# Kernel tuning notes

Hardware: AMD Instinct MI355X
Metric: run time of the kernel (lower is better)

## Reference

```python
import jax, jax.numpy as jnp
import numpy as np

N_NODES = 50000
N_EDGES = 800000
IN_DIM = 128
HIDDEN = 256
N_CLASSES = 16
N_GRAPHS = 128


def setup_inputs() -> dict:
    key = jax.random.key(0)
    ks = jax.random.split(key, 10)
    x = jax.random.normal(ks[0], (N_NODES, IN_DIM), dtype=jnp.float32)
    edge_index = jax.random.randint(ks[1], (2, N_EDGES), 0, N_NODES, dtype=jnp.int64)
    batch = jnp.sort(jax.random.randint(ks[2], (N_NODES,), 0, N_GRAPHS, dtype=jnp.int64))
    s = 1.0 / np.sqrt(HIDDEN)
    return {
        "x": x,
        "edge_index": edge_index,
        "batch": batch,
        "W_in": jax.random.normal(ks[3], (IN_DIM, HIDDEN), dtype=jnp.float32) / np.sqrt(IN_DIM),
        "b_in": jnp.zeros((HIDDEN,), dtype=jnp.float32),
        "W1": jax.random.normal(ks[4], (HIDDEN, HIDDEN), dtype=jnp.float32) * s,
        "b1": jnp.zeros((HIDDEN,), dtype=jnp.float32),
        "W2": jax.random.normal(ks[5], (HIDDEN, HIDDEN), dtype=jnp.float32) * s,
        "b2": jnp.zeros((HIDDEN,), dtype=jnp.float32),
        "W_out": jax.random.normal(ks[6], (HIDDEN, N_CLASSES), dtype=jnp.float32) * s,
        "b_out": jnp.zeros((N_CLASSES,), dtype=jnp.float32),
    }


def gcn_conv(x, W, b, src, dst):
    # PyG GCNConv: add self-loops, symmetric norm D^-1/2 A D^-1/2, scatter-add at target.
    h = x @ W  # [N, H]
    n = x.shape[0]
    # degree of target nodes, including one self-loop per node
    deg = jax.ops.segment_sum(jnp.ones_like(dst, dtype=h.dtype), dst, num_segments=n) + 1.0
    dinv = deg ** -0.5  # [N]
    norm = dinv[src] * dinv[dst]  # [E]
    msg = h[src] * norm[:, None]  # [E, H]  gather + scale
    agg = jax.ops.segment_sum(msg, dst, num_segments=n)  # scatter-add
    agg = agg + h * (dinv * dinv)[:, None]  # self-loop contribution
    return agg + b


def reference(x, edge_index, batch, W_in, b_in, W1, b1, W2, b2, W_out, b_out):
    src, dst = edge_index[0], edge_index[1]
    h = x @ W_in + b_in
    # layer 1 (dropout is identity in eval mode)
    h = jax.nn.relu(gcn_conv(h, W1, b1, src, dst))
    # layer 2
    h = jax.nn.relu(gcn_conv(h, W2, b2, src, dst))
    # global mean pool over graphs
    sums = jax.ops.segment_sum(h, batch, num_segments=N_GRAPHS)  # [G, H]
    counts = jax.ops.segment_sum(jnp.ones((h.shape[0],), h.dtype), batch, num_segments=N_GRAPHS)
    pooled = sums / jnp.maximum(counts, 1.0)[:, None]
    return pooled @ W_out + b_out  # [G, n_classes]
```

## Files before the change

### kernel.cpp

```cpp
#include <hip/hip_runtime.h>
#include <hip/hip_bf16.h>

typedef __attribute__((ext_vector_type(8))) short bf16x8;
typedef __attribute__((ext_vector_type(4))) float f32x4;

__device__ __forceinline__ unsigned short f2bf(float f) {
    unsigned u = __float_as_uint(f);
    u += 0x7fff + ((u >> 16) & 1);
    return (unsigned short)(u >> 16);
}
__device__ __forceinline__ float bf2f(unsigned short s) {
    return __uint_as_float(((unsigned)s) << 16);
}

#define GL2LDS16(g, l) __builtin_amdgcn_global_load_lds(                      \
        (const __attribute__((address_space(1))) void*)(g),                   \
        (__attribute__((address_space(3))) void*)(l), 16, 0, 0)


__global__ __launch_bounds__(256) void fused_misc_kernel(
        const int* __restrict__ dst, int* __restrict__ cnt, int e,
        const float* __restrict__ W2, unsigned short* __restrict__ Wt2,
        const float* __restrict__ x, unsigned short* __restrict__ xb, int n4,
        int CB, int TB) {
    int b = blockIdx.x;
    if (b < CB) {
        int i = b * 256 + threadIdx.x;
        if (i < e) atomicAdd(&cnt[dst[i]], 1);
    } else if (b < CB + TB) {
        int i = (b - CB) * 256 + threadIdx.x;
        int k = i >> 8, n = i & 255;
        Wt2[(size_t)n * 256 + k] = f2bf(W2[i]);
    } else {
        int i = (b - CB - TB) * 256 + threadIdx.x;
        if (i < n4) {
            float4 v = ((const float4*)x)[i];
            ushort4 o;
            o.x = f2bf(v.x); o.y = f2bf(v.y); o.z = f2bf(v.z); o.w = f2bf(v.w);
            ((ushort4*)xb)[i] = o;
        }
    }
}


__global__ __launch_bounds__(256) void wfuse_kernel(const float* __restrict__ W_in,
                                                    const float* __restrict__ b_in,
                                                    const float* __restrict__ W1,
                                                    unsigned short* __restrict__ WfT,
                                                    float* __restrict__ bv) {
    __shared__ float row[256];
    int k = blockIdx.x;
    int n = threadIdx.x;
    row[n] = (k < 128) ? W_in[k * 256 + n] : b_in[n];
    __syncthreads();
    float acc = 0.f;
    #pragma unroll 4
    for (int j = 0; j < 256; ++j) acc = fmaf(row[j], W1[j * 256 + n], acc);
    if (k < 128) WfT[(size_t)n * 128 + k] = f2bf(acc);
    else bv[n] = acc;
}


__global__ __launch_bounds__(256) void block_sum_kernel(const int* __restrict__ cnt,
                                                        int* __restrict__ bsums, int n) {
    int tid = threadIdx.x;
    int i = blockIdx.x * 256 + tid;
    int v = (i < n) ? cnt[i] : 0;
    #pragma unroll
    for (int off = 32; off > 0; off >>= 1) v += __shfl_down(v, off);
    __shared__ int ws[4];
    if ((tid & 63) == 0) ws[tid >> 6] = v;
    __syncthreads();
    if (tid == 0) bsums[blockIdx.x] = ws[0] + ws[1] + ws[2] + ws[3];
}

__global__ __launch_bounds__(256) void scatter_scan_kernel(const int* __restrict__ cnt,
                                                           const int* __restrict__ bsums,
                                                           int* __restrict__ offsets,
                                                           int* __restrict__ cursor,
                                                           float* __restrict__ dinv,
                                                           int n, int nb) {
    int tid = threadIdx.x;
    int lane = tid & 63, wid = tid >> 6;
    __shared__ int ws[4], wp[4];

    int bv = (tid < nb && tid < (int)blockIdx.x) ? bsums[tid] : 0;
    int br = bv;
    #pragma unroll
    for (int off = 32; off > 0; off >>= 1) br += __shfl_down(br, off);
    if (lane == 0) wp[wid] = br;

    int i = blockIdx.x * 256 + tid;
    int v = (i < n) ? cnt[i] : 0;
    int s = v;
    #pragma unroll
    for (int off = 1; off < 64; off <<= 1) {
        int t = __shfl_up(s, off);
        if (lane >= off) s += t;
    }
    if (lane == 63) ws[wid] = s;
    __syncthreads();
    int wo = 0;
    #pragma unroll
    for (int k = 0; k < 4; ++k) wo += (k < wid) ? ws[k] : 0;
    int bpref = wp[0] + wp[1] + wp[2] + wp[3];
    int excl = bpref + wo + s - v;
    if (i <= n) { offsets[i] = excl; }
    if (i < n) {
        cursor[i] = excl;
        dinv[i] = rsqrtf((float)v + 1.0f);
    }
}

__global__ void fill_kernel(const int* __restrict__ src, const int* __restrict__ dst,
                            int* __restrict__ cursor, int* __restrict__ csr, int e) {
    int i = blockIdx.x * blockDim.x + threadIdx.x;
    if (i < e) {
        int p = atomicAdd(&cursor[dst[i]], 1);
        csr[p] = src[i];
    }
}


template <int MODE>
__global__ __launch_bounds__(256) void gemm_bf16(const unsigned short* __restrict__ A,
                                                 const unsigned short* __restrict__ Wt,
                                                 const float* __restrict__ aux,
                                                 const float* __restrict__ aux2,
                                                 const float* __restrict__ aux3,
                                                 unsigned short* __restrict__ C,
                                                 int M, int K) {
    __shared__ unsigned short As[128 * 64];
    __shared__ unsigned short Bs[128 * 64];
    const int tid  = threadIdx.x;
    const int lane = tid & 63;
    const int w    = tid >> 6;
    const int wr   = w >> 1, wc = w & 1;
    const int row0 = blockIdx.x * 128;
    const int col0 = blockIdx.y * 128;
    const int mlane = lane & 15, quad = lane >> 4;

    f32x4 acc[4][4];
    #pragma unroll
    for (int i = 0; i < 4; ++i)
        #pragma unroll
        for (int j = 0; j < 4; ++j) acc[i][j] = f32x4{0.f, 0.f, 0.f, 0.f};

    const unsigned short* gA[4]; const unsigned short* gB[4];
    unsigned short* lA[4]; unsigned short* lB[4];
    #pragma unroll
    for (int p = 0; p < 4; ++p) {
        int cid = (p * 4 + w) * 64 + lane;
        int row = cid >> 3, slot = cid & 7;
        int rowA = row0 + row; if (rowA >= M) rowA = M - 1;
        gA[p] = A + (size_t)rowA * K + slot * 8;
        gB[p] = Wt + (size_t)(col0 + row) * K + slot * 8;
        lA[p] = &As[((p * 4 + w) * 64) * 8];
        lB[p] = &Bs[((p * 4 + w) * 64) * 8];
    }

    for (int k0 = 0; k0 < K; k0 += 64) {
        #pragma unroll
        for (int p = 0; p < 4; ++p) GL2LDS16(gA[p] + k0, lA[p]);
        #pragma unroll
        for (int p = 0; p < 4; ++p) GL2LDS16(gB[p] + k0, lB[p]);
        __syncthreads();
        #pragma unroll
        for (int ks = 0; ks < 2; ++ks) {
            bf16x8 af[4], bfv[4];
            #pragma unroll
            for (int i = 0; i < 4; ++i)
                af[i] = *(const bf16x8*)&As[(wr * 64 + i * 16 + mlane) * 64 + ks * 32 + quad * 8];
            #pragma unroll
            for (int j = 0; j < 4; ++j)
                bfv[j] = *(const bf16x8*)&Bs[(wc * 64 + j * 16 + mlane) * 64 + ks * 32 + quad * 8];
            #pragma unroll
            for (int i = 0; i < 4; ++i)
                #pragma unroll
                for (int j = 0; j < 4; ++j)
                    acc[i][j] = __builtin_amdgcn_mfma_f32_16x16x32_bf16(af[i], bfv[j], acc[i][j], 0, 0, 0);
        }
        __syncthreads();
    }

    float bj[4], cj[4];
    if (MODE == 0) {
        #pragma unroll
        for (int j = 0; j < 4; ++j) bj[j] = aux[col0 + wc * 64 + j * 16 + mlane];
    } else if (MODE == 2) {
        #pragma unroll
        for (int j = 0; j < 4; ++j) {
            int gcol = col0 + wc * 64 + j * 16 + mlane;
            bj[j] = aux2[gcol];
            cj[j] = aux3[gcol];
        }
    }
    #pragma unroll
    for (int i = 0; i < 4; ++i) {
        #pragma unroll
        for (int r = 0; r < 4; ++r) {
            int grow = row0 + wr * 64 + i * 16 + quad * 4 + r;
            if (grow < M) {
                float d = (MODE != 0) ? aux[grow] : 0.f;
                #pragma unroll
                for (int j = 0; j < 4; ++j) {
                    int gcol = col0 + wc * 64 + j * 16 + mlane;
                    float v = acc[i][j][r];
                    if (MODE == 0)      v = v + bj[j];
                    else if (MODE == 1) v = v * d;
                    else {              v = fmaf(d, bj[j], v) + cj[j]; v = fmaxf(v, 0.f); }
                    C[(size_t)grow * 256 + gcol] = f2bf(v);
                }
            }
        }
    }
}


__global__ __launch_bounds__(256) void agg_x_kernel(const unsigned short* __restrict__ xb,
                                                    const int* __restrict__ offsets,
                                                    const int* __restrict__ csr,
                                                    const float* __restrict__ dinv,
                                                    unsigned short* __restrict__ ax,
                                                    float* __restrict__ s_out, int n) {
    int node = blockIdx.x * 4 + (threadIdx.x >> 6);
    if (node >= n) return;
    int lane = threadIdx.x & 63;
    int half = lane >> 5, hl = lane & 31;
    const ushort4* x4 = (const ushort4*)xb;
    int beg = offsets[node], end = offsets[node + 1];
    float dn = dinv[node];
    float a0 = 0.f, a1 = 0.f, a2 = 0.f, a3 = 0.f;
    float sdl = 0.f;
    int e = beg;
    while (e < end) {
        int cnt = end - e; if (cnt > 64) cnt = 64;
        int myi = 0; float mydv = 0.f;
        if (lane < cnt) { myi = csr[e + lane]; mydv = dinv[myi]; sdl += mydv; }
        int j = 0;
        for (; j + 8 <= cnt; j += 8) {
            int s0 = __shfl(myi, j + half),     s1 = __shfl(myi, j + 2 + half);
            int s2 = __shfl(myi, j + 4 + half), s3 = __shfl(myi, j + 6 + half);
            float d0 = __shfl(mydv, j + half),     d1 = __shfl(mydv, j + 2 + half);
            float d2 = __shfl(mydv, j + 4 + half), d3 = __shfl(mydv, j + 6 + half);
            ushort4 v0 = x4[(size_t)s0 * 32 + hl];
            ushort4 v1 = x4[(size_t)s1 * 32 + hl];
            ushort4 v2 = x4[(size_t)s2 * 32 + hl];
            ushort4 v3 = x4[(size_t)s3 * 32 + hl];
            a0 = fmaf(bf2f(v0.x), d0, a0); a1 = fmaf(bf2f(v0.y), d0, a1);
            a2 = fmaf(bf2f(v0.z), d0, a2); a3 = fmaf(bf2f(v0.w), d0, a3);
            a0 = fmaf(bf2f(v1.x), d1, a0); a1 = fmaf(bf2f(v1.y), d1, a1);
            a2 = fmaf(bf2f(v1.z), d1, a2); a3 = fmaf(bf2f(v1.w), d1, a3);
            a0 = fmaf(bf2f(v2.x), d2, a0); a1 = fmaf(bf2f(v2.y), d2, a1);
            a2 = fmaf(bf2f(v2.z), d2, a2); a3 = fmaf(bf2f(v2.w), d2, a3);
            a0 = fmaf(bf2f(v3.x), d3, a0); a1 = fmaf(bf2f(v3.y), d3, a1);
            a2 = fmaf(bf2f(v3.z), d3, a2); a3 = fmaf(bf2f(v3.w), d3, a3);
        }
        for (; j < cnt; j += 2) {
            int jj = j + half; int sel = (jj < cnt) ? jj : j;
            int s_ = __shfl(myi, sel);
            float dd = __shfl(mydv, sel);
            if (jj >= cnt) dd = 0.f;
            ushort4 v = x4[(size_t)s_ * 32 + hl];
            a0 = fmaf(bf2f(v.x), dd, a0); a1 = fmaf(bf2f(v.y), dd, a1);
            a2 = fmaf(bf2f(v.z), dd, a2); a3 = fmaf(bf2f(v.w), dd, a3);
        }
        e += cnt;
    }
    a0 += __shfl_xor(a0, 32); a1 += __shfl_xor(a1, 32);
    a2 += __shfl_xor(a2, 32); a3 += __shfl_xor(a3, 32);
    float sd = sdl;
    #pragma unroll
    for (int off = 32; off > 0; off >>= 1) sd += __shfl_down(sd, off);
    if (lane < 32) {
        ushort4 sv = x4[(size_t)node * 32 + hl];
        a0 = fmaf(dn, bf2f(sv.x), a0) * dn;
        a1 = fmaf(dn, bf2f(sv.y), a1) * dn;
        a2 = fmaf(dn, bf2f(sv.z), a2) * dn;
        a3 = fmaf(dn, bf2f(sv.w), a3) * dn;
        ushort4 r;
        r.x = f2bf(a0); r.y = f2bf(a1); r.z = f2bf(a2); r.w = f2bf(a3);
        ((ushort4*)ax)[(size_t)node * 32 + hl] = r;
        if (lane == 0) s_out[node] = dn * (sd + dn);
    }
}


__global__ __launch_bounds__(256) void agg_kernel(const unsigned short* __restrict__ hs,
                                                  const int* __restrict__ offsets,
                                                  const int* __restrict__ csr,
                                                  const float* __restrict__ dinv,
                                                  const float* __restrict__ bias,
                                                  unsigned short* __restrict__ out, int n) {
    int node = blockIdx.x * 4 + (threadIdx.x >> 6);
    if (node >= n) return;
    int lane = threadIdx.x & 63;
    const ushort4* hs4 = (const ushort4*)hs;
    int beg = offsets[node], end = offsets[node + 1];
    ushort4 sv = hs4[(size_t)node * 64 + lane];
    float a0 = bf2f(sv.x), a1 = bf2f(sv.y), a2 = bf2f(sv.z), a3 = bf2f(sv.w);
    float c0 = 0.f, c1 = 0.f, c2 = 0.f, c3 = 0.f;

    int e = beg;
    while (e < end) {
        int cnt = end - e; if (cnt > 64) cnt = 64;
        int myi = (lane < cnt) ? csr[e + lane] : 0;
        int j = 0;
        for (; j + 8 <= cnt; j += 8) {
            int s0 = __shfl(myi, j + 0), s1 = __shfl(myi, j + 1);
            int s2 = __shfl(myi, j + 2), s3 = __shfl(myi, j + 3);
            int s4 = __shfl(myi, j + 4), s5 = __shfl(myi, j + 5);
            int s6 = __shfl(myi, j + 6), s7 = __shfl(myi, j + 7);
            ushort4 v0 = hs4[(size_t)s0 * 64 + lane];
            ushort4 v1 = hs4[(size_t)s1 * 64 + lane];
            ushort4 v2 = hs4[(size_t)s2 * 64 + lane];
            ushort4 v3 = hs4[(size_t)s3 * 64 + lane];
            ushort4 v4 = hs4[(size_t)s4 * 64 + lane];
            ushort4 v5 = hs4[(size_t)s5 * 64 + lane];
            ushort4 v6 = hs4[(size_t)s6 * 64 + lane];
            ushort4 v7 = hs4[(size_t)s7 * 64 + lane];
            a0 += bf2f(v0.x) + bf2f(v1.x) + bf2f(v2.x) + bf2f(v3.x);
            a1 += bf2f(v0.y) + bf2f(v1.y) + bf2f(v2.y) + bf2f(v3.y);
            a2 += bf2f(v0.z) + bf2f(v1.z) + bf2f(v2.z) + bf2f(v3.z);
            a3 += bf2f(v0.w) + bf2f(v1.w) + bf2f(v2.w) + bf2f(v3.w);
            c0 += bf2f(v4.x) + bf2f(v5.x) + bf2f(v6.x) + bf2f(v7.x);
            c1 += bf2f(v4.y) + bf2f(v5.y) + bf2f(v6.y) + bf2f(v7.y);
            c2 += bf2f(v4.z) + bf2f(v5.z) + bf2f(v6.z) + bf2f(v7.z);
            c3 += bf2f(v4.w) + bf2f(v5.w) + bf2f(v6.w) + bf2f(v7.w);
        }
        for (; j < cnt; ++j) {
            int s = __shfl(myi, j);
            ushort4 v = hs4[(size_t)s * 64 + lane];
            a0 += bf2f(v.x); a1 += bf2f(v.y); a2 += bf2f(v.z); a3 += bf2f(v.w);
        }
        e += cnt;
    }
    a0 += c0; a1 += c1; a2 += c2; a3 += c3;

    float d = dinv[node];
    float4 b = ((const float4*)bias)[lane];
    ushort4 r;
    r.x = f2bf(fmaxf(fmaf(a0, d, b.x), 0.f));
    r.y = f2bf(fmaxf(fmaf(a1, d, b.y), 0.f));
    r.z = f2bf(fmaxf(fmaf(a2, d, b.z), 0.f));
    r.w = f2bf(fmaxf(fmaf(a3, d, b.w), 0.f));
    ((ushort4*)out)[(size_t)node * 64 + lane] = r;
}


__global__ __launch_bounds__(256) void pool_partial_kernel(const unsigned short* __restrict__ h,
                                                           const int* __restrict__ batch,
                                                           float* __restrict__ sums,
                                                           int* __restrict__ counts,
                                                           int n, int chunk) {
    int beg = blockIdx.x * chunk;
    int end = beg + chunk; if (end > n) end = n;
    if (beg >= end) return;
    int c = threadIdx.x;
    int curg = batch[beg];
    float acc = 0.f;
    int runlen = 0;
    for (int i = beg; i < end; ++i) {
        int g = batch[i];
        if (g != curg) {
            atomicAdd(&sums[(size_t)curg * 256 + c], acc);
            if (c == 0) atomicAdd(&counts[curg], runlen);
            acc = 0.f; runlen = 0; curg = g;
        }
        acc += bf2f(h[(size_t)i * 256 + c]);
        ++runlen;
    }
    atomicAdd(&sums[(size_t)curg * 256 + c], acc);
    if (c == 0) atomicAdd(&counts[curg], runlen);
}

__global__ __launch_bounds__(256) void pool_final_kernel(const float* __restrict__ sums,
                                                         const int* __restrict__ counts,
                                                         const float* __restrict__ Wout,
                                                         const float* __restrict__ bout,
                                                         float* __restrict__ out) {
    __shared__ float pl[256];
    int g = blockIdx.x;
    int c = threadIdx.x;
    int cnt = counts[g];
    pl[c] = sums[(size_t)g * 256 + c] / (float)(cnt > 0 ? cnt : 1);
    __syncthreads();
    if (c < 16) {
        float o = bout[c];
        #pragma unroll 4
        for (int k = 0; k < 256; ++k) o = fmaf(pl[k], Wout[k * 16 + c], o);
        out[g * 16 + c] = o;
    }
}


extern "C" void kernel_launch(void* const* d_in, const int* in_sizes, int n_in,
                              void* d_out, int out_size, void* d_ws, size_t ws_size,
                              hipStream_t stream) {
    const float* x     = (const float*)d_in[0];
    const int*   ei    = (const int*)d_in[1];
    const int*   batch = (const int*)d_in[2];
    const float* W_in  = (const float*)d_in[3];
    const float* b_in  = (const float*)d_in[4];
    const float* W1    = (const float*)d_in[5];
    const float* b1    = (const float*)d_in[6];
    const float* W2    = (const float*)d_in[7];
    const float* b2    = (const float*)d_in[8];
    const float* Wout  = (const float*)d_in[9];
    const float* bout  = (const float*)d_in[10];

    const int E = in_sizes[1] / 2;
    const int N = in_sizes[2];
    const int IN_DIM = in_sizes[0] / N;
    const int G = 128;
    const int* src = ei;
    const int* dst = ei + E;

    char* ws = (char*)d_ws;
    size_t off = 0;
    auto alloc = [&](size_t bytes) { size_t p = off; off += (bytes + 255) & ~(size_t)255; return p; };
    unsigned short* bufA = (unsigned short*)(ws + alloc((size_t)N * 256 * 2));
    unsigned short* bufB = (unsigned short*)(ws + alloc((size_t)N * 256 * 2));
    unsigned short* xb   = (unsigned short*)(ws + alloc((size_t)N * IN_DIM * 2));
    unsigned short* Wt2  = (unsigned short*)(ws + alloc((size_t)256 * 256 * 2));
    unsigned short* WfT  = (unsigned short*)(ws + alloc((size_t)256 * IN_DIM * 2));
    float*          bv   = (float*)(ws + alloc((size_t)256 * 4));
    float*          sbuf = (float*)(ws + alloc((size_t)N * 4));
    size_t zbeg = off;
    int*   deg_cnt = (int*)(ws + alloc((size_t)N * 4));
    float* sums    = (float*)(ws + alloc((size_t)G * 256 * 4));
    int*   counts  = (int*)(ws + alloc((size_t)G * 4));
    size_t zend = off;
    float* dinv    = (float*)(ws + alloc((size_t)N * 4));
    int*   offsets = (int*)(ws + alloc((size_t)(N + 1) * 4));
    int*   cursor  = (int*)(ws + alloc((size_t)N * 4));
    int*   csr     = (int*)(ws + alloc((size_t)E * 4));
    int*   bsums   = (int*)(ws + alloc((size_t)256 * 4));
    (void)ws_size;

    unsigned short* axb = bufB;

    const int NB  = (N + 255) / 256;
    const int NB1 = (N + 1 + 255) / 256;
    const int CB  = (E + 255) / 256;
    const int TB  = (256 * 256 + 255) / 256;
    const int XB  = (N * IN_DIM / 4 + 255) / 256;

    hipMemsetAsync(ws + zbeg, 0, zend - zbeg, stream);
    fused_misc_kernel<<<CB + TB + XB, 256, 0, stream>>>(
        dst, deg_cnt, E, W2, Wt2, x, xb, N * IN_DIM / 4, CB, TB);
    wfuse_kernel<<<129, 256, 0, stream>>>(W_in, b_in, W1, WfT, bv);
    block_sum_kernel<<<NB, 256, 0, stream>>>(deg_cnt, bsums, N);
    scatter_scan_kernel<<<NB1, 256, 0, stream>>>(deg_cnt, bsums, offsets, cursor, dinv, N, NB);
    fill_kernel<<<(E + 255) / 256, 256, 0, stream>>>(src, dst, cursor, csr, E);

    agg_x_kernel<<<(N + 3) / 4, 256, 0, stream>>>(xb, offsets, csr, dinv, axb, sbuf, N);
    dim3 gg((N + 127) / 128, 2);
    gemm_bf16<2><<<gg, 256, 0, stream>>>(axb, WfT, sbuf, bv, b1, bufA, N, IN_DIM);

    gemm_bf16<1><<<gg, 256, 0, stream>>>(bufA, Wt2, dinv, nullptr, nullptr, bufB, N, 256);
    agg_kernel<<<(N + 3) / 4, 256, 0, stream>>>(bufB, offsets, csr, dinv, b2, bufA, N);

    const int PBLOCKS = 512;
    int chunk = (N + PBLOCKS - 1) / PBLOCKS;
    pool_partial_kernel<<<PBLOCKS, 256, 0, stream>>>(bufA, batch, sums, counts, N, chunk);
    pool_final_kernel<<<G, 256, 0, stream>>>(sums, counts, Wout, bout, (float*)d_out);
}
```

Measured before the change: 380.4 us.

## Use 16-bit CSR indices, slice second aggregation by columns, fold wfuse into misc kernel

Stores CSR source indices as unsigned short instead of int, which halves index traffic. This only works because N_NODES (50000) fits in 16 bits, so it breaks for larger graphs. The layer-2 aggregation is rewritten to split the 256 feature columns into 8 slices across blocks. Each wavefront processes 8 edges at once with 8 lanes per edge, followed by a shuffle reduction, and uses nontemporal loads and stores. The weight-fusion kernel is also merged into the fused misc launch to save one kernel launch.

Result: slower. 473.6 us (+24.5%).

```diff
diff --git a/kernel.cpp b/kernel.cpp
--- a/kernel.cpp
+++ b/kernel.cpp
@@ -1,5 +1,6 @@
 #include <hip/hip_runtime.h>
 #include <hip/hip_bf16.h>
+#include <string.h>
 
 typedef __attribute__((ext_vector_type(8))) short bf16x8;
 typedef __attribute__((ext_vector_type(4))) float f32x4;
@@ -22,16 +23,20 @@
         const int* __restrict__ dst, int* __restrict__ cnt, int e,
         const float* __restrict__ W2, unsigned short* __restrict__ Wt2,
         const float* __restrict__ x, unsigned short* __restrict__ xb, int n4,
-        int CB, int TB) {
+        const float* __restrict__ W_in, const float* __restrict__ b_in,
+        const float* __restrict__ W1,
+        unsigned short* __restrict__ WfT, float* __restrict__ bv,
+        int CB, int TB, int XB) {
+    __shared__ float row[256];
     int b = blockIdx.x;
     if (b < CB) {
         int i = b * 256 + threadIdx.x;
         if (i < e) atomicAdd(&cnt[dst[i]], 1);
     } else if (b < CB + TB) {
         int i = (b - CB) * 256 + threadIdx.x;
-        int k = i >> 8, n = i & 255;
-        Wt2[(size_t)n * 256 + k] = f2bf(W2[i]);
-    } else {
+        int k = i >> 8, nn = i & 255;
+        Wt2[(size_t)nn * 256 + k] = f2bf(W2[i]);
+    } else if (b < CB + TB + XB) {
         int i = (b - CB - TB) * 256 + threadIdx.x;
         if (i < n4) {
             float4 v = ((const float4*)x)[i];
@@ -39,25 +44,17 @@
             o.x = f2bf(v.x); o.y = f2bf(v.y); o.z = f2bf(v.z); o.w = f2bf(v.w);
             ((ushort4*)xb)[i] = o;
         }
-    }
-}
-
-
-__global__ __launch_bounds__(256) void wfuse_kernel(const float* __restrict__ W_in,
-                                                    const float* __restrict__ b_in,
-                                                    const float* __restrict__ W1,
-                                                    unsigned short* __restrict__ WfT,
-                                                    float* __restrict__ bv) {
-    __shared__ float row[256];
-    int k = blockIdx.x;
-    int n = threadIdx.x;
-    row[n] = (k < 128) ? W_in[k * 256 + n] : b_in[n];
-    __syncthreads();
-    float acc = 0.f;
-    #pragma unroll 4
-    for (int j = 0; j < 256; ++j) acc = fmaf(row[j], W1[j * 256 + n], acc);
-    if (k < 128) WfT[(size_t)n * 128 + k] = f2bf(acc);
-    else bv[n] = acc;
+    } else {
+        int k = b - (CB + TB + XB);
+        int nn = threadIdx.x;
+        row[nn] = (k < 128) ? W_in[k * 256 + nn] : b_in[nn];
+        __syncthreads();
+        float acc = 0.f;
+        #pragma unroll 4
+        for (int j = 0; j < 256; ++j) acc = fmaf(row[j], W1[j * 256 + nn], acc);
+        if (k < 128) WfT[(size_t)nn * 128 + k] = f2bf(acc);
+        else bv[nn] = acc;
+    }
 }
 
 
@@ -113,11 +110,12 @@
 }
 
 __global__ void fill_kernel(const int* __restrict__ src, const int* __restrict__ dst,
-                            int* __restrict__ cursor, int* __restrict__ csr, int e) {
+                            int* __restrict__ cursor, unsigned short* __restrict__ csr16,
+                            int e) {
     int i = blockIdx.x * blockDim.x + threadIdx.x;
     if (i < e) {
         int p = atomicAdd(&cursor[dst[i]], 1);
-        csr[p] = src[i];
+        csr16[p] = (unsigned short)src[i];
     }
 }
 
@@ -219,7 +217,7 @@
 
 __global__ __launch_bounds__(256) void agg_x_kernel(const unsigned short* __restrict__ xb,
                                                     const int* __restrict__ offsets,
-                                                    const int* __restrict__ csr,
+                                                    const unsigned short* __restrict__ csr16,
                                                     const float* __restrict__ dinv,
                                                     unsigned short* __restrict__ ax,
                                                     float* __restrict__ s_out, int n) {
@@ -236,7 +234,7 @@
     while (e < end) {
         int cnt = end - e; if (cnt > 64) cnt = 64;
         int myi = 0; float mydv = 0.f;
-        if (lane < cnt) { myi = csr[e + lane]; mydv = dinv[myi]; sdl += mydv; }
+        if (lane < cnt) { myi = (int)csr16[e + lane]; mydv = dinv[myi]; sdl += mydv; }
         int j = 0;
         for (; j + 8 <= cnt; j += 8) {
             int s0 = __shfl(myi, j + half),     s1 = __shfl(myi, j + 2 + half);
@@ -286,65 +284,57 @@
 }
 
 
-__global__ __launch_bounds__(256) void agg_kernel(const unsigned short* __restrict__ hs,
-                                                  const int* __restrict__ offsets,
-                                                  const int* __restrict__ csr,
-                                                  const float* __restrict__ dinv,
-                                                  const float* __restrict__ bias,
-                                                  unsigned short* __restrict__ out, int n) {
-    int node = blockIdx.x * 4 + (threadIdx.x >> 6);
+__global__ __launch_bounds__(256) void agg_slice_kernel(const unsigned short* __restrict__ hs,
+                                                        const int* __restrict__ offsets,
+                                                        const unsigned short* __restrict__ csr16,
+                                                        const float* __restrict__ dinv,
+                                                        const float* __restrict__ bias,
+                                                        unsigned short* __restrict__ out, int n) {
+    int s = blockIdx.x & 7;
+    int node = (blockIdx.x >> 3) * 4 + (threadIdx.x >> 6);
     if (node >= n) return;
     int lane = threadIdx.x & 63;
+    int esub = lane >> 3, c4 = lane & 7;
     const ushort4* hs4 = (const ushort4*)hs;
+    const int sbase = s * 8 + c4;
     int beg = offsets[node], end = offsets[node + 1];
-    ushort4 sv = hs4[(size_t)node * 64 + lane];
-    float a0 = bf2f(sv.x), a1 = bf2f(sv.y), a2 = bf2f(sv.z), a3 = bf2f(sv.w);
-    float c0 = 0.f, c1 = 0.f, c2 = 0.f, c3 = 0.f;
-
-    int e = beg;
-    while (e < end) {
-        int cnt = end - e; if (cnt > 64) cnt = 64;
-        int myi = (lane < cnt) ? csr[e + lane] : 0;
-        int j = 0;
-        for (; j + 8 <= cnt; j += 8) {
-            int s0 = __shfl(myi, j + 0), s1 = __shfl(myi, j + 1);
-            int s2 = __shfl(myi, j + 2), s3 = __shfl(myi, j + 3);
-            int s4 = __shfl(myi, j + 4), s5 = __shfl(myi, j + 5);
-            int s6 = __shfl(myi, j + 6), s7 = __shfl(myi, j + 7);
-            ushort4 v0 = hs4[(size_t)s0 * 64 + lane];
-            ushort4 v1 = hs4[(size_t)s1 * 64 + lane];
-            ushort4 v2 = hs4[(size_t)s2 * 64 + lane];
-            ushort4 v3 = hs4[(size_t)s3 * 64 + lane];
-            ushort4 v4 = hs4[(size_t)s4 * 64 + lane];
-            ushort4 v5 = hs4[(size_t)s5 * 64 + lane];
-            ushort4 v6 = hs4[(size_t)s6 * 64 + lane];
-            ushort4 v7 = hs4[(size_t)s7 * 64 + lane];
-            a0 += bf2f(v0.x) + bf2f(v1.x) + bf2f(v2.x) + bf2f(v3.x);
-            a1 += bf2f(v0.y) + bf2f(v1.y) + bf2f(v2.y) + bf2f(v3.y);
-            a2 += bf2f(v0.z) + bf2f(v1.z) + bf2f(v2.z) + bf2f(v3.z);
-            a3 += bf2f(v0.w) + bf2f(v1.w) + bf2f(v2.w) + bf2f(v3.w);
-            c0 += bf2f(v4.x) + bf2f(v5.x) + bf2f(v6.x) + bf2f(v7.x);
-            c1 += bf2f(v4.y) + bf2f(v5.y) + bf2f(v6.y) + bf2f(v7.y);
-            c2 += bf2f(v4.z) + bf2f(v5.z) + bf2f(v6.z) + bf2f(v7.z);
-            c3 += bf2f(v4.w) + bf2f(v5.w) + bf2f(v6.w) + bf2f(v7.w);
-        }
-        for (; j < cnt; ++j) {
-            int s = __shfl(myi, j);
-            ushort4 v = hs4[(size_t)s * 64 + lane];
-            a0 += bf2f(v.x); a1 += bf2f(v.y); a2 += bf2f(v.z); a3 += bf2f(v.w);
-        }
-        e += cnt;
-    }
-    a0 += c0; a1 += c1; a2 += c2; a3 += c3;
-
-    float d = dinv[node];
-    float4 b = ((const float4*)bias)[lane];
-    ushort4 r;
-    r.x = f2bf(fmaxf(fmaf(a0, d, b.x), 0.f));
-    r.y = f2bf(fmaxf(fmaf(a1, d, b.y), 0.f));
-    r.z = f2bf(fmaxf(fmaf(a2, d, b.z), 0.f));
-    r.w = f2bf(fmaxf(fmaf(a3, d, b.w), 0.f));
-    ((ushort4*)out)[(size_t)node * 64 + lane] = r;
+    float a0 = 0.f, a1 = 0.f, a2 = 0.f, a3 = 0.f;
+
+    for (int e = beg; e < end; e += 64) {
+        int cend = end - e; if (cend > 64) cend = 64;
+        int myi = (lane < cend) ? (int)__builtin_nontemporal_load(&csr16[e + lane]) : 0;
+        for (int j = 0; j < cend; j += 8) {
+            int slot = j + esub;
+            int src = __shfl(myi, slot);
+            float w = (slot < cend) ? 1.0f : 0.0f;
+            ushort4 v = hs4[(size_t)src * 64 + sbase];
+            a0 = fmaf(bf2f(v.x), w, a0);
+            a1 = fmaf(bf2f(v.y), w, a1);
+            a2 = fmaf(bf2f(v.z), w, a2);
+            a3 = fmaf(bf2f(v.w), w, a3);
+        }
+    }
+    a0 += __shfl_xor(a0, 8);  a1 += __shfl_xor(a1, 8);
+    a2 += __shfl_xor(a2, 8);  a3 += __shfl_xor(a3, 8);
+    a0 += __shfl_xor(a0, 16); a1 += __shfl_xor(a1, 16);
+    a2 += __shfl_xor(a2, 16); a3 += __shfl_xor(a3, 16);
+    a0 += __shfl_xor(a0, 32); a1 += __shfl_xor(a1, 32);
+    a2 += __shfl_xor(a2, 32); a3 += __shfl_xor(a3, 32);
+
+    if (esub == 0) {
+        ushort4 sv = hs4[(size_t)node * 64 + sbase];
+        float d = dinv[node];
+        float4 b = ((const float4*)bias)[sbase];
+        ushort4 r;
+        r.x = f2bf(fmaxf(fmaf(a0 + bf2f(sv.x), d, b.x), 0.f));
+        r.y = f2bf(fmaxf(fmaf(a1 + bf2f(sv.y), d, b.y), 0.f));
+        r.z = f2bf(fmaxf(fmaf(a2 + bf2f(sv.z), d, b.z), 0.f));
+        r.w = f2bf(fmaxf(fmaf(a3 + bf2f(sv.w), d, b.w), 0.f));
+        unsigned long long rv;
+        memcpy(&rv, &r, 8);
+        __builtin_nontemporal_store(rv,
+            (unsigned long long*)&((ushort4*)out)[(size_t)node * 64 + sbase]);
+    }
 }
 
 
@@ -434,7 +424,7 @@
     float* dinv    = (float*)(ws + alloc((size_t)N * 4));
     int*   offsets = (int*)(ws + alloc((size_t)(N + 1) * 4));
     int*   cursor  = (int*)(ws + alloc((size_t)N * 4));
-    int*   csr     = (int*)(ws + alloc((size_t)E * 4));
+    unsigned short* csr16 = (unsigned short*)(ws + alloc((size_t)E * 2));
     int*   bsums   = (int*)(ws + alloc((size_t)256 * 4));
     (void)ws_size;
 
@@ -445,21 +435,22 @@
     const int CB  = (E + 255) / 256;
     const int TB  = (256 * 256 + 255) / 256;
     const int XB  = (N * IN_DIM / 4 + 255) / 256;
+    const int WB  = 129;
 
     hipMemsetAsync(ws + zbeg, 0, zend - zbeg, stream);
-    fused_misc_kernel<<<CB + TB + XB, 256, 0, stream>>>(
-        dst, deg_cnt, E, W2, Wt2, x, xb, N * IN_DIM / 4, CB, TB);
-    wfuse_kernel<<<129, 256, 0, stream>>>(W_in, b_in, W1, WfT, bv);
+    fused_misc_kernel<<<CB + TB + XB + WB, 256, 0, stream>>>(
+        dst, deg_cnt, E, W2, Wt2, x, xb, N * IN_DIM / 4,
+        W_in, b_in, W1, WfT, bv, CB, TB, XB);
     block_sum_kernel<<<NB, 256, 0, stream>>>(deg_cnt, bsums, N);
     scatter_scan_kernel<<<NB1, 256, 0, stream>>>(deg_cnt, bsums, offsets, cursor, dinv, N, NB);
-    fill_kernel<<<(E + 255) / 256, 256, 0, stream>>>(src, dst, cursor, csr, E);
-
-    agg_x_kernel<<<(N + 3) / 4, 256, 0, stream>>>(xb, offsets, csr, dinv, axb, sbuf, N);
+    fill_kernel<<<(E + 255) / 256, 256, 0, stream>>>(src, dst, cursor, csr16, E);
+
+    agg_x_kernel<<<(N + 3) / 4, 256, 0, stream>>>(xb, offsets, csr16, dinv, axb, sbuf, N);
     dim3 gg((N + 127) / 128, 2);
     gemm_bf16<2><<<gg, 256, 0, stream>>>(axb, WfT, sbuf, bv, b1, bufA, N, IN_DIM);
 
     gemm_bf16<1><<<gg, 256, 0, stream>>>(bufA, Wt2, dinv, nullptr, nullptr, bufB, N, 256);
-    agg_kernel<<<(N + 3) / 4, 256, 0, stream>>>(bufB, offsets, csr, dinv, b2, bufA, N);
+    agg_slice_kernel<<<((N + 3) / 4) * 8, 256, 0, stream>>>(bufB, offsets, csr16, dinv, b2, bufA, N);
 
     const int PBLOCKS = 512;
     int chunk = (N + PBLOCKS - 1) / PBLOCKS;
```
